# Kernel tuning notes

Hardware: AMD Instinct MI355X
Metric: run time of the kernel (lower is better)

## Reference

```python
import jax, jax.numpy as jnp
import numpy as np

P = 16                     # patch size
D = 192                    # embed dim (forced by SAT d_model=192)
NHEAD = 3                  # ViT-Tiny heads
SAT_H, SAT_DK, SAT_DV = 8, 32, 32
N_SLICE = 10
PER_LI = jnp.linspace(0.1, 1.0, N_SLICE)
LN_EPS = 1e-5


def layernorm(z, g, b):
    m = z.mean(-1, keepdims=True)
    v = ((z - m) ** 2).mean(-1, keepdims=True)
    return (z - m) * jax.lax.rsqrt(v + LN_EPS) * g + b


def setup_inputs() -> dict:
    key = jax.random.key(0)
    ks = jax.random.split(key, 32)
    B, IMG, DEPTH, MLP = 128, 224, 12, 4 * D
    S = (IMG // P) ** 2 + 1  # 197 tokens
    n = lambda k, sh: jax.random.normal(k, sh, jnp.float32) * 0.02
    z = lambda sh: jnp.zeros(sh, jnp.float32)
    o = lambda sh: jnp.ones(sh, jnp.float32)
    return {
        "x": jax.random.uniform(ks[0], (B, 3, IMG, IMG), jnp.float32),
        "x_g_norm": jax.random.uniform(ks[1], (B, 1, 56, 56), jnp.float32),
        "patch_w": n(ks[2], (D, 3, P, P)), "patch_b": z((D,)),
        "cls_token": n(ks[3], (1, 1, D)), "pos_embed": n(ks[4], (1, S, D)),
        "eleva_embed": n(ks[5], (1, D)),
        "sat_wq": n(ks[6], (D, SAT_H * SAT_DK)), "sat_bq": z((SAT_H * SAT_DK,)),
        "sat_wk": n(ks[7], (D, SAT_H * SAT_DK)), "sat_bk": z((SAT_H * SAT_DK,)),
        "sat_wv": n(ks[8], (D, SAT_H * SAT_DV)), "sat_bv": z((SAT_H * SAT_DV,)),
        "sat_wo": n(ks[9], (SAT_H * SAT_DV, D)), "sat_bo": z((D,)),
        "ln1_g": o((DEPTH, D)), "ln1_b": z((DEPTH, D)),
        "qkv_w": n(ks[10], (DEPTH, D, 3 * D)), "qkv_b": z((DEPTH, 3 * D)),
        "proj_w": n(ks[11], (DEPTH, D, D)), "proj_b": z((DEPTH, D)),
        "ln2_g": o((DEPTH, D)), "ln2_b": z((DEPTH, D)),
        "fc1_w": n(ks[12], (DEPTH, D, MLP)), "fc1_b": z((DEPTH, MLP)),
        "fc2_w": n(ks[13], (DEPTH, MLP, D)), "fc2_b": z((DEPTH, D)),
        "norm_g": o((D,)), "norm_b": z((D,)),
    }


def _forward(x, x_g_norm, patch_w, patch_b, cls_token, pos_embed, eleva_embed,
             sat_wq, sat_bq, sat_wk, sat_bk, sat_wv, sat_bv, sat_wo, sat_bo,
             ln1_g, ln1_b, qkv_w, qkv_b, proj_w, proj_b, ln2_g, ln2_b,
             fc1_w, fc1_b, fc2_w, fc2_b, norm_g, norm_b):
    B = x.shape[0]
    # --- patch embed: Conv2d(3, D, kernel=P, stride=P) -> [B, N, D] ---
    feat = jax.lax.conv_general_dilated(
        x, patch_w, (P, P), 'VALID', dimension_numbers=('NCHW', 'OIHW', 'NCHW'))
    feat = feat + patch_b[None, :, None, None]
    tokens = feat.reshape(B, D, -1).transpose(0, 2, 1)          # [B, 196, D]
    tok = jnp.concatenate([jnp.broadcast_to(cls_token, (B, 1, D)), tokens], axis=1)
    tok = tok + pos_embed                                        # [B, S, D]
    S = tok.shape[1]
    # --- elevation weight per sample (vectorized bisect + linear interp) ---
    means = x_g_norm.mean(axis=(1, 2, 3))                        # [B]
    idx = jnp.clip(jnp.searchsorted(PER_LI, means, side='left'), 0, N_SLICE - 1)
    per_hi = PER_LI[idx]
    per_lo = jnp.where(idx == 0, 0.0, PER_LI[jnp.maximum(idx - 1, 0)])
    idx_f = idx.astype(jnp.float32)
    idx_inter = idx_f - (per_hi - means) / (per_hi - per_lo)
    w = jnp.where(idx == N_SLICE - 1, idx_f, idx_inter) / N_SLICE  # [B]
    # --- SAT fusion: per (batch, token) a 2-element attention over (token, ele) ---
    ele = jnp.broadcast_to(eleva_embed[0] * w[:, None, None], tok.shape)  # [B,S,D]
    at_in = jnp.stack([tok, ele], axis=2)                        # [B, S, 2, D]
    q = (at_in @ sat_wq + sat_bq).reshape(B, S, 2, SAT_H, SAT_DK)
    k = (at_in @ sat_wk + sat_bk).reshape(B, S, 2, SAT_H, SAT_DK)
    v = (at_in @ sat_wv + sat_bv).reshape(B, S, 2, SAT_H, SAT_DV)
    att = jnp.einsum('bsqhd,bskhd->bshqk', q, k) * (1.0 / np.sqrt(SAT_DK))
    att = jax.nn.softmax(att, axis=-1)
    sat_o = jnp.einsum('bshqk,bskhd->bsqhd', att, v).reshape(B, S, 2, SAT_H * SAT_DV)
    sat_o = sat_o @ sat_wo + sat_bo                              # [B, S, 2, D]
    h = sat_o[..., 0, :] + sat_o[..., 1, :]                      # [B, S, D]
    # --- ViT blocks via scan over stacked layer params ---
    hd = D // NHEAD

    def block(z, p):
        l1g, l1b, qw, qb, pw, pb, l2g, l2b, f1w, f1b, f2w, f2b = p
        y = layernorm(z, l1g, l1b)
        qkv = y @ qw + qb                                        # [B, S, 3D]
        q_, k_, v_ = jnp.split(qkv, 3, axis=-1)
        q_ = q_.reshape(B, S, NHEAD, hd)
        k_ = k_.reshape(B, S, NHEAD, hd)
        v_ = v_.reshape(B, S, NHEAD, hd)
        a = jnp.einsum('bqhd,bkhd->bhqk', q_, k_) * (hd ** -0.5)
        a = jax.nn.softmax(a, axis=-1)
        o = jnp.einsum('bhqk,bkhd->bqhd', a, v_).reshape(B, S, D)
        z = z + o @ pw + pb
        y = layernorm(z, l2g, l2b)
        z = z + jax.nn.gelu(y @ f1w + f1b, approximate=False) @ f2w + f2b
        return z, None

    h, _ = jax.lax.scan(block, h, (ln1_g, ln1_b, qkv_w, qkv_b, proj_w, proj_b,
                                   ln2_g, ln2_b, fc1_w, fc1_b, fc2_w, fc2_b))
    h = layernorm(h, norm_g, norm_b)
    return h[:, 0]                                               # [B, D] cls token


def reference(x, x_g_norm, patch_w, patch_b, cls_token, pos_embed, eleva_embed,
              sat_wq, sat_bq, sat_wk, sat_bk, sat_wv, sat_bv, sat_wo, sat_bo,
              ln1_g, ln1_b, qkv_w, qkv_b, proj_w, proj_b, ln2_g, ln2_b,
              fc1_w, fc1_b, fc2_w, fc2_b, norm_g, norm_b):
    return _forward(x, x_g_norm, patch_w, patch_b, cls_token, pos_embed, eleva_embed,
                    sat_wq, sat_bq, sat_wk, sat_bk, sat_wv, sat_bv, sat_wo, sat_bo,
                    ln1_g, ln1_b, qkv_w, qkv_b, proj_w, proj_b, ln2_g, ln2_b,
                    fc1_w, fc1_b, fc2_w, fc2_b, norm_g, norm_b)
```

## Files before the change

### kernel.cpp

```cpp
#include <hip/hip_runtime.h>


#define BATCH 128
#define SEQ 197
#define BS_ROWS (BATCH * SEQ)
#define DMODEL 192
#define NPATCH 196
#define MROWS_PATCH (BATCH * NPATCH)
#define KPATCH 768
#define MLPDIM 768
#define DEPTH 12
#define SPAD 224

typedef float f32x4 __attribute__((ext_vector_type(4)));
typedef short s16x8 __attribute__((ext_vector_type(8)));

__device__ __forceinline__ float wredSum(float v) {
#pragma unroll
  for (int o = 32; o > 0; o >>= 1) v += __shfl_xor(v, o, 64);
  return v;
}

__device__ __forceinline__ unsigned short f2bf(float f) {
  union { float f; unsigned u; } v;
  v.f = f;
  unsigned r = v.u + 0x7FFFu + ((v.u >> 16) & 1u);
  return (unsigned short)(r >> 16);
}
__device__ __forceinline__ float bf2f(unsigned short u) {
  union { unsigned u; float f; } v;
  v.u = ((unsigned)u) << 16;
  return v.f;
}

__global__ __launch_bounds__(256) void eleva_w_kernel(const float* __restrict__ xg,
                                                      float* __restrict__ wout) {
  const int b = blockIdx.x;
  const float* p = xg + (size_t)b * 3136;
  float s = 0.f;
  for (int i = threadIdx.x; i < 3136; i += 256) s += p[i];
  __shared__ float partial[4];
  s = wredSum(s);
  if ((threadIdx.x & 63) == 0) partial[threadIdx.x >> 6] = s;
  __syncthreads();
  if (threadIdx.x == 0) {
    float m = (partial[0] + partial[1] + partial[2] + partial[3]) / 3136.f;
    int idx = 0;
#pragma unroll
    for (int i = 0; i < 10; i++) {
      float pv = 0.1f * (float)(i + 1);
      if (pv < m) idx = i + 1;
    }
    if (idx > 9) idx = 9;
    float wv;
    if (idx == 9) {
      wv = 9.f;
    } else {
      float hi = 0.1f * (float)(idx + 1);
      float lo = (idx == 0) ? 0.f : 0.1f * (float)idx;
      wv = (float)idx - (hi - m) / (hi - lo);
    }
    wout[b] = wv / 10.f;
  }
}

__global__ __launch_bounds__(256) void wtrans_kernel(const float* __restrict__ in,
                                                     unsigned short* __restrict__ out,
                                                     int R, int C) {
  const int z = blockIdx.z;
  in += (size_t)z * R * C;
  out += (size_t)z * R * C;
  const int c0 = blockIdx.x * 32, r0 = blockIdx.y * 32;
  __shared__ float t[32][33];
  const int tr = threadIdx.x >> 3, tc = (threadIdx.x & 7) * 4;
  const float4 v = *(const float4*)(in + (size_t)(r0 + tr) * C + c0 + tc);
  t[tr][tc] = v.x; t[tr][tc + 1] = v.y; t[tr][tc + 2] = v.z; t[tr][tc + 3] = v.w;
  __syncthreads();
  ushort4 o;
  o.x = f2bf(t[tc + 0][tr]);
  o.y = f2bf(t[tc + 1][tr]);
  o.z = f2bf(t[tc + 2][tr]);
  o.w = f2bf(t[tc + 3][tr]);
  *(ushort4*)(out + (size_t)(c0 + tr) * R + r0 + tc) = o;
}

__global__ __launch_bounds__(256) void convert_kernel(const float* __restrict__ in,
                                                      unsigned short* __restrict__ out, int n4) {
  const int i = blockIdx.x * 256 + threadIdx.x;
  if (i >= n4) return;
  const float4 v = *(const float4*)(in + (size_t)i * 4);
  ushort4 o;
  o.x = f2bf(v.x); o.y = f2bf(v.y); o.z = f2bf(v.z); o.w = f2bf(v.w);
  *(ushort4*)(out + (size_t)i * 4) = o;
}

__global__ __launch_bounds__(256) void im2col_kernel(const float* __restrict__ x,
                                                     unsigned short* __restrict__ col) {
  const int i = blockIdx.x * 256 + threadIdx.x;
  if (i >= MROWS_PATCH * KPATCH) return;
  const int k = i % KPATCH, row = i / KPATCH;
  const int b = row / NPATCH, p = row % NPATCH;
  const int py = p / 14, px = p % 14;
  const int c = k >> 8, r = (k >> 4) & 15, cc = k & 15;
  col[i] = f2bf(x[(((size_t)b * 3 + c) * 224 + (py * 16 + r)) * 224 + (px * 16 + cc)]);
}

__global__ __launch_bounds__(256) void assemble_kernel(const unsigned short* __restrict__ tok_raw,
                                                       const float* __restrict__ cls,
                                                       const float* __restrict__ pos,
                                                       float* __restrict__ H,
                                                       unsigned short* __restrict__ Hbf) {
  const int i = blockIdx.x * 256 + threadIdx.x;
  if (i >= BS_ROWS * DMODEL) return;
  const int d = i % DMODEL, row = i / DMODEL;
  const int b = row / SEQ, s = row % SEQ;
  float v;
  if (s == 0)
    v = cls[d] + pos[d];
  else
    v = bf2f(tok_raw[(size_t)(b * NPATCH + s - 1) * DMODEL + d]) + pos[(size_t)s * DMODEL + d];
  H[i] = v;
  Hbf[i] = f2bf(v);
}

__global__ __launch_bounds__(256) void ele_proj_kernel(
    const float* __restrict__ ele_emb, const float* __restrict__ wq, const float* __restrict__ bq,
    const float* __restrict__ wk, const float* __restrict__ bk,
    const float* __restrict__ wv, const float* __restrict__ bv,
    const float* __restrict__ wvec, float* __restrict__ eq, float* __restrict__ ek,
    float* __restrict__ ev) {
  const int b = blockIdx.x, t = threadIdx.x;
  __shared__ float es[DMODEL];
  if (t < DMODEL) es[t] = ele_emb[t] * wvec[b];
  __syncthreads();
  float aq = bq[t], ak = bk[t], av = bv[t];
  for (int d = 0; d < DMODEL; d++) {
    const float e = es[d];
    aq += e * wq[d * 256 + t];
    ak += e * wk[d * 256 + t];
    av += e * wv[d * 256 + t];
  }
  eq[b * 256 + t] = aq;
  ek[b * 256 + t] = ak;
  ev[b * 256 + t] = av;
}

__global__ __launch_bounds__(256) void sat_mix_kernel(
    const unsigned short* __restrict__ qt, const unsigned short* __restrict__ kt,
    const unsigned short* __restrict__ vt, const float* __restrict__ eq,
    const float* __restrict__ ek, const float* __restrict__ ev,
    unsigned short* __restrict__ o256) {
  const int gid = blockIdx.x * 256 + threadIdx.x;
  const int tok = gid >> 3, h = gid & 7;
  if (tok >= BS_ROWS) return;
  const int b = tok / SEQ;
  const unsigned short* qp = qt + (size_t)tok * 256 + h * 32;
  const unsigned short* kp = kt + (size_t)tok * 256 + h * 32;
  const unsigned short* vp = vt + (size_t)tok * 256 + h * 32;
  const float* eqp = eq + b * 256 + h * 32;
  const float* ekp = ek + b * 256 + h * 32;
  const float* evp = ev + b * 256 + h * 32;
  float s00 = 0.f, s01 = 0.f, s10 = 0.f, s11 = 0.f;
#pragma unroll 8
  for (int d = 0; d < 32; d++) {
    const float q_ = bf2f(qp[d]), k_ = bf2f(kp[d]), eq_ = eqp[d], ek_ = ekp[d];
    s00 += q_ * k_;
    s01 += q_ * ek_;
    s10 += eq_ * k_;
    s11 += eq_ * ek_;
  }
  const float sc = 0.17677669529663687f;
  s00 *= sc; s01 *= sc; s10 *= sc; s11 *= sc;
  const float m0 = fmaxf(s00, s01), m1 = fmaxf(s10, s11);
  const float e00 = __expf(s00 - m0), e01 = __expf(s01 - m0);
  const float e10 = __expf(s10 - m1), e11 = __expf(s11 - m1);
  const float w0 = e00 / (e00 + e01) + e10 / (e10 + e11);
  const float w1 = e01 / (e00 + e01) + e11 / (e10 + e11);
  unsigned short* op = o256 + (size_t)tok * 256 + h * 32;
#pragma unroll 8
  for (int d = 0; d < 32; d++) op[d] = f2bf(w0 * bf2f(vp[d]) + w1 * evp[d]);
}

template <int BK, int EPI>
__global__ __launch_bounds__(256) void gemm_mfma(const unsigned short* __restrict__ A,
                                                 const unsigned short* __restrict__ Bt,
                                                 const float* __restrict__ bias,
                                                 const float* __restrict__ res,
                                                 void* __restrict__ Cout, int M, int N, int K) {
  constexpr int SLOTS = BK / 8;
  __shared__ unsigned short As[128 * BK];
  __shared__ unsigned short Bs[64 * BK];
  const int tid = threadIdx.x, lane = tid & 63, w = tid >> 6;
  const int n0 = blockIdx.x * 64;
  const int m0 = blockIdx.y * 128;
  const int c = lane & 15, g = lane >> 4;
  const int wm = (w >> 1) * 64, wn = (w & 1) * 32;
  f32x4 acc[4][2] = {};
  for (int k0 = 0; k0 < K; k0 += BK) {
    if (k0) __syncthreads();
    constexpr int AI = 32 * SLOTS / 64;
#pragma unroll
    for (int it = 0; it < AI; it++) {
      const int s = it * 64 + lane;
      const int r = w * 32 + s / SLOTS;
      const int col = s % SLOTS;
      const int scol = col ^ (r & 7);
      const unsigned short* gp = A + (size_t)(m0 + r) * K + k0 + scol * 8;
      __builtin_amdgcn_global_load_lds(
          (const __attribute__((address_space(1))) unsigned int*)gp,
          (__attribute__((address_space(3))) unsigned int*)(As + ((size_t)(w * 32) * SLOTS + it * 64) * 8),
          16, 0, 0);
    }
    constexpr int BI = 16 * SLOTS / 64;
#pragma unroll
    for (int it = 0; it < BI; it++) {
      const int s = it * 64 + lane;
      const int r = w * 16 + s / SLOTS;
      const int col = s % SLOTS;
      const int scol = col ^ (r & 7);
      const unsigned short* gp = Bt + (size_t)(n0 + r) * K + k0 + scol * 8;
      __builtin_amdgcn_global_load_lds(
          (const __attribute__((address_space(1))) unsigned int*)gp,
          (__attribute__((address_space(3))) unsigned int*)(Bs + ((size_t)(w * 16) * SLOTS + it * 64) * 8),
          16, 0, 0);
    }
    __syncthreads();
#pragma unroll
    for (int kk = 0; kk < BK / 32; kk++) {
      const int sw = ((kk * 4 + g) ^ (c & 7)) << 3;
      s16x8 af[4], bfr[2];
#pragma unroll
      for (int i = 0; i < 4; i++) af[i] = *(const s16x8*)&As[(wm + i * 16 + c) * BK + sw];
#pragma unroll
      for (int j = 0; j < 2; j++) bfr[j] = *(const s16x8*)&Bs[(wn + j * 16 + c) * BK + sw];
#pragma unroll
      for (int i = 0; i < 4; i++)
#pragma unroll
        for (int j = 0; j < 2; j++)
          acc[i][j] = __builtin_amdgcn_mfma_f32_16x16x32_bf16(af[i], bfr[j], acc[i][j], 0, 0, 0);
    }
  }
  const int ncol0 = n0 + wn + c;
  float b0 = bias[ncol0], b1 = bias[ncol0 + 16];
  if (EPI == 3) { b0 *= 2.f; b1 *= 2.f; }
#pragma unroll
  for (int i = 0; i < 4; i++) {
#pragma unroll
    for (int r_ = 0; r_ < 4; r_++) {
      const size_t m = m0 + wm + i * 16 + g * 4 + r_;
#pragma unroll
      for (int j = 0; j < 2; j++) {
        float v = acc[i][j][r_] + (j ? b1 : b0);
        const size_t idx = m * N + ncol0 + j * 16;
        if (EPI == 0) {
          ((unsigned short*)Cout)[idx] = f2bf(v);
        } else if (EPI == 1) {
          v = 0.5f * v * (1.0f + erff(v * 0.70710678118654752f));
          ((unsigned short*)Cout)[idx] = f2bf(v);
        } else if (EPI == 2) {
          ((float*)Cout)[idx] = v + res[idx];
        } else {
          ((float*)Cout)[idx] = v;
        }
      }
    }
  }
}

__global__ __launch_bounds__(256) void ln_kernel(const float* __restrict__ X,
                                                 const float* __restrict__ g,
                                                 const float* __restrict__ bta,
                                                 unsigned short* __restrict__ Y, int nrows) {
  const int w = threadIdx.x >> 6, lane = threadIdx.x & 63;
  const int row = blockIdx.x * 4 + w;
  if (row >= nrows) return;
  const float* x = X + (size_t)row * DMODEL;
  const float x0 = x[lane], x1 = x[lane + 64], x2 = x[lane + 128];
  const float m = wredSum(x0 + x1 + x2) * (1.f / 192.f);
  const float d0 = x0 - m, d1 = x1 - m, d2 = x2 - m;
  const float v = wredSum(d0 * d0 + d1 * d1 + d2 * d2) * (1.f / 192.f);
  const float inv = rsqrtf(v + 1e-5f);
  unsigned short* y = Y + (size_t)row * DMODEL;
  y[lane] = f2bf(d0 * inv * g[lane] + bta[lane]);
  y[lane + 64] = f2bf(d1 * inv * g[lane + 64] + bta[lane + 64]);
  y[lane + 128] = f2bf(d2 * inv * g[lane + 128] + bta[lane + 128]);
}

__global__ __launch_bounds__(256) void final_ln_kernel(const float* __restrict__ H,
                                                       const float* __restrict__ g,
                                                       const float* __restrict__ bta,
                                                       float* __restrict__ out) {
  const int w = threadIdx.x >> 6, lane = threadIdx.x & 63;
  const int bi = blockIdx.x * 4 + w;
  if (bi >= BATCH) return;
  const float* x = H + (size_t)bi * SEQ * DMODEL;
  const float x0 = x[lane], x1 = x[lane + 64], x2 = x[lane + 128];
  const float m = wredSum(x0 + x1 + x2) * (1.f / 192.f);
  const float d0 = x0 - m, d1 = x1 - m, d2 = x2 - m;
  const float v = wredSum(d0 * d0 + d1 * d1 + d2 * d2) * (1.f / 192.f);
  const float inv = rsqrtf(v + 1e-5f);
  float* y = out + (size_t)bi * DMODEL;
  y[lane] = d0 * inv * g[lane] + bta[lane];
  y[lane + 64] = d1 * inv * g[lane + 64] + bta[lane + 64];
  y[lane + 128] = d2 * inv * g[lane + 128] + bta[lane + 128];
}

__global__ __launch_bounds__(256) void vtrans_kernel(const unsigned short* __restrict__ qkv,
                                                     unsigned short* __restrict__ vt) {
  const int bid = blockIdx.x;
  const int sc = bid & 3, bh = bid >> 2;
  const int b = bh / 3, h = bh % 3;
  const int s0 = sc * 64;
  __shared__ unsigned short t[64][72];
  const int tid = threadIdx.x;
  for (int e = tid; e < 64 * 64; e += 256) {
    const int sp = e >> 6, d = e & 63;
    const int s = s0 + sp;
    t[sp][d] = (s < SEQ) ? qkv[((size_t)(b * SEQ + s)) * 576 + 384 + h * 64 + d] : (unsigned short)0;
  }
  __syncthreads();
  for (int e = tid; e < 64 * 64; e += 256) {
    const int d = e >> 6, sp = e & 63;
    const int s = s0 + sp;
    if (s < SPAD) vt[((size_t)bh * 64 + d) * SPAD + s] = t[sp][d];
  }
}

__global__ __launch_bounds__(64) void attn_mfma_kernel(const unsigned short* __restrict__ qkv,
                                                       const unsigned short* __restrict__ vt,
                                                       unsigned short* __restrict__ out) {
  const int bid = blockIdx.x;
  const int bh = bid / 13, qt = bid % 13;
  const int b = bh / 3, h = bh % 3;
  const int row0 = b * SEQ;
  const int q0 = qt * 16;
  const int lane = threadIdx.x;
  const int c = lane & 15, g = lane >> 4;

  __shared__ __attribute__((aligned(16))) unsigned short P[16][232];

  const int qr = row0 + min(q0 + c, SEQ - 1);
  const unsigned short* qp = qkv + (size_t)qr * 576 + h * 64 + g * 8;
  const s16x8 qlo = *(const s16x8*)qp;
  const s16x8 qhi = *(const s16x8*)(qp + 32);

  f32x4 acc[13];
#pragma unroll
  for (int t = 0; t < 13; t++) {
    const int kr = row0 + min(t * 16 + c, SEQ - 1);
    const unsigned short* kp = qkv + (size_t)kr * 576 + 192 + h * 64 + g * 8;
    const s16x8 klo = *(const s16x8*)kp;
    const s16x8 khi = *(const s16x8*)(kp + 32);
    f32x4 z = {0.f, 0.f, 0.f, 0.f};
    z = __builtin_amdgcn_mfma_f32_16x16x32_bf16(qlo, klo, z, 0, 0, 0);
    acc[t] = __builtin_amdgcn_mfma_f32_16x16x32_bf16(qhi, khi, z, 0, 0, 0);
  }

  const bool m12 = (c >= 5);
#pragma unroll
  for (int r = 0; r < 4; r++) {
    float mx = -INFINITY;
#pragma unroll
    for (int t = 0; t < 13; t++) {
      const float v = (t == 12 && m12) ? -INFINITY : acc[t][r];
      mx = fmaxf(mx, v);
    }
#pragma unroll
    for (int o = 1; o <= 8; o <<= 1) mx = fmaxf(mx, __shfl_xor(mx, o, 64));
    const float ms = mx * 0.125f;
    float sum = 0.f;
#pragma unroll
    for (int t = 0; t < 13; t++) {
      const float e = (t == 12 && m12) ? 0.f : __expf(acc[t][r] * 0.125f - ms);
      acc[t][r] = e;
      sum += e;
    }
#pragma unroll
    for (int o = 1; o <= 8; o <<= 1) sum += __shfl_xor(sum, o, 64);
    const float inv = 1.f / sum;
#pragma unroll
    for (int t = 0; t < 13; t++) P[g * 4 + r][t * 16 + c] = f2bf(acc[t][r] * inv);
  }
  {
    unsigned short z4[4] = {0, 0, 0, 0};
    *(uint2*)&P[c][208 + g * 4] = *(uint2*)z4;
  }
  __builtin_amdgcn_s_waitcnt(0);

  f32x4 oacc[4];
#pragma unroll
  for (int dt = 0; dt < 4; dt++) oacc[dt] = (f32x4){0.f, 0.f, 0.f, 0.f};
  const unsigned short* vbase = vt + (size_t)bh * 64 * SPAD;
#pragma unroll
  for (int ch = 0; ch < 7; ch++) {
    const s16x8 pa = *(const s16x8*)&P[c][ch * 32 + g * 8];
#pragma unroll
    for (int dt = 0; dt < 4; dt++) {
      const s16x8 vb = *(const s16x8*)(vbase + (size_t)(dt * 16 + c) * SPAD + ch * 32 + g * 8);
      oacc[dt] = __builtin_amdgcn_mfma_f32_16x16x32_bf16(pa, vb, oacc[dt], 0, 0, 0);
    }
  }

#pragma unroll
  for (int dt = 0; dt < 4; dt++) {
#pragma unroll
    for (int r = 0; r < 4; r++) {
      const int q = q0 + g * 4 + r;
      if (q < SEQ) out[(size_t)(row0 + q) * DMODEL + h * 64 + dt * 16 + c] = f2bf(oacc[dt][r]);
    }
  }
}

extern "C" void kernel_launch(void* const* d_in, const int* in_sizes, int n_in,
                              void* d_out, int out_size, void* d_ws, size_t ws_size,
                              hipStream_t stream) {
  const float* x       = (const float*)d_in[0];
  const float* xg      = (const float*)d_in[1];
  const float* patch_w = (const float*)d_in[2];
  const float* patch_b = (const float*)d_in[3];
  const float* cls_tok = (const float*)d_in[4];
  const float* pos_emb = (const float*)d_in[5];
  const float* ele_emb = (const float*)d_in[6];
  const float* sat_wq  = (const float*)d_in[7];
  const float* sat_bq  = (const float*)d_in[8];
  const float* sat_wk  = (const float*)d_in[9];
  const float* sat_bk  = (const float*)d_in[10];
  const float* sat_wv  = (const float*)d_in[11];
  const float* sat_bv  = (const float*)d_in[12];
  const float* sat_wo  = (const float*)d_in[13];
  const float* sat_bo  = (const float*)d_in[14];
  const float* ln1_g   = (const float*)d_in[15];
  const float* ln1_b   = (const float*)d_in[16];
  const float* qkv_w   = (const float*)d_in[17];
  const float* qkv_b   = (const float*)d_in[18];
  const float* proj_w  = (const float*)d_in[19];
  const float* proj_b  = (const float*)d_in[20];
  const float* ln2_g   = (const float*)d_in[21];
  const float* ln2_b   = (const float*)d_in[22];
  const float* fc1_w   = (const float*)d_in[23];
  const float* fc1_b   = (const float*)d_in[24];
  const float* fc2_w   = (const float*)d_in[25];
  const float* fc2_b   = (const float*)d_in[26];
  const float* norm_g  = (const float*)d_in[27];
  const float* norm_b  = (const float*)d_in[28];
  float* out = (float*)d_out;
  float* ws = (float*)d_ws;

  float* W_ELE = ws;
  float* EQ = ws + 256;
  float* EK = EQ + 32768;
  float* EV = EK + 32768;
  float* H = ws + 98560;
  unsigned short* Hbf   = (unsigned short*)(ws + 4940032);
  unsigned short* Ybf   = (unsigned short*)(ws + 7360768);
  unsigned short* QKVbf = (unsigned short*)(ws + 9781504);
  unsigned short* MLPbf = (unsigned short*)(ws + 17043712);
  unsigned short* VTB   = (unsigned short*)(ws + 26726656);
  unsigned short* WTS   = (unsigned short*)(ws + 29479168);

  unsigned short* qkv_wt   = WTS;
  unsigned short* proj_wt  = WTS + 1327104;
  unsigned short* fc1_wt   = WTS + 1769472;
  unsigned short* fc2_wt   = WTS + 3538944;
  unsigned short* patch_bf = WTS + 5308416;
  unsigned short* satq_t   = WTS + 5455872;
  unsigned short* satk_t   = WTS + 5505024;
  unsigned short* satv_t   = WTS + 5554176;
  unsigned short* sato_t   = WTS + 5603328;

  unsigned short* COLbf  = MLPbf;
  unsigned short* TOKRAW = Ybf;
  unsigned short* QTbf   = QKVbf;
  unsigned short* KTbf   = QKVbf + 6455296;
  unsigned short* VTbf   = MLPbf;
  unsigned short* O256bf = MLPbf + 6455296;

  wtrans_kernel<<<dim3(18, 6, 12), 256, 0, stream>>>(qkv_w, qkv_wt, 192, 576);
  wtrans_kernel<<<dim3(6, 6, 12), 256, 0, stream>>>(proj_w, proj_wt, 192, 192);
  wtrans_kernel<<<dim3(24, 6, 12), 256, 0, stream>>>(fc1_w, fc1_wt, 192, 768);
  wtrans_kernel<<<dim3(6, 24, 12), 256, 0, stream>>>(fc2_w, fc2_wt, 768, 192);
  wtrans_kernel<<<dim3(8, 6, 1), 256, 0, stream>>>(sat_wq, satq_t, 192, 256);
  wtrans_kernel<<<dim3(8, 6, 1), 256, 0, stream>>>(sat_wk, satk_t, 192, 256);
  wtrans_kernel<<<dim3(8, 6, 1), 256, 0, stream>>>(sat_wv, satv_t, 192, 256);
  wtrans_kernel<<<dim3(6, 8, 1), 256, 0, stream>>>(sat_wo, sato_t, 256, 192);
  convert_kernel<<<144, 256, 0, stream>>>(patch_w, patch_bf, 36864);

  eleva_w_kernel<<<BATCH, 256, 0, stream>>>(xg, W_ELE);

  im2col_kernel<<<(MROWS_PATCH * KPATCH) / 256, 256, 0, stream>>>(x, COLbf);
  gemm_mfma<192, 0><<<dim3(3, 196), 256, 0, stream>>>(COLbf, patch_bf, patch_b, nullptr,
                                                      TOKRAW, MROWS_PATCH, DMODEL, KPATCH);
  assemble_kernel<<<(BS_ROWS * DMODEL) / 256, 256, 0, stream>>>(TOKRAW, cls_tok, pos_emb, H, Hbf);

  ele_proj_kernel<<<BATCH, 256, 0, stream>>>(ele_emb, sat_wq, sat_bq, sat_wk, sat_bk,
                                             sat_wv, sat_bv, W_ELE, EQ, EK, EV);
  gemm_mfma<192, 0><<<dim3(4, 197), 256, 0, stream>>>(Hbf, satq_t, sat_bq, nullptr, QTbf,
                                                      BS_ROWS, 256, DMODEL);
  gemm_mfma<192, 0><<<dim3(4, 197), 256, 0, stream>>>(Hbf, satk_t, sat_bk, nullptr, KTbf,
                                                      BS_ROWS, 256, DMODEL);
  gemm_mfma<192, 0><<<dim3(4, 197), 256, 0, stream>>>(Hbf, satv_t, sat_bv, nullptr, VTbf,
                                                      BS_ROWS, 256, DMODEL);
  sat_mix_kernel<<<BS_ROWS / 32, 256, 0, stream>>>(QTbf, KTbf, VTbf, EQ, EK, EV, O256bf);
  gemm_mfma<128, 3><<<dim3(3, 197), 256, 0, stream>>>(O256bf, sato_t, sat_bo, nullptr, H,
                                                      BS_ROWS, DMODEL, 256);

  for (int l = 0; l < DEPTH; l++) {
    ln_kernel<<<BS_ROWS / 4, 256, 0, stream>>>(H, ln1_g + l * DMODEL, ln1_b + l * DMODEL, Ybf,
                                               BS_ROWS);
    gemm_mfma<192, 0><<<dim3(9, 197), 256, 0, stream>>>(
        Ybf, qkv_wt + (size_t)l * 110592, qkv_b + l * 576, nullptr, QKVbf, BS_ROWS, 576, DMODEL);
    vtrans_kernel<<<BATCH * 3 * 4, 256, 0, stream>>>(QKVbf, VTB);
    attn_mfma_kernel<<<BATCH * 3 * 13, 64, 0, stream>>>(QKVbf, VTB, Ybf);
    gemm_mfma<192, 2><<<dim3(3, 197), 256, 0, stream>>>(
        Ybf, proj_wt + (size_t)l * 36864, proj_b + l * DMODEL, H, H, BS_ROWS, DMODEL, DMODEL);
    ln_kernel<<<BS_ROWS / 4, 256, 0, stream>>>(H, ln2_g + l * DMODEL, ln2_b + l * DMODEL, Ybf,
                                               BS_ROWS);
    gemm_mfma<192, 1><<<dim3(12, 197), 256, 0, stream>>>(
        Ybf, fc1_wt + (size_t)l * 147456, fc1_b + l * MLPDIM, nullptr, MLPbf, BS_ROWS, MLPDIM,
        DMODEL);
    gemm_mfma<192, 2><<<dim3(3, 197), 256, 0, stream>>>(
        MLPbf, fc2_wt + (size_t)l * 147456, fc2_b + l * DMODEL, H, H, BS_ROWS, DMODEL, MLPDIM);
  }

  final_ln_kernel<<<BATCH / 4, 256, 0, stream>>>(H, norm_g, norm_b, out);
}
```

Before: 2.011 ms.

## Double-buffer GEMM with 128x96 tiles, fuse SAT QKV and patch assembly

The MFMA GEMM now uses BK=64 with two LDS buffers, so the next K-slice loads while the current one computes. Tiles widen from 64 to 96 columns, which changes every grid shape. The three SAT Q/K/V projections are merged into one N=768 GEMM with concatenated weights and biases. The patch-embed GEMM epilogue writes H and Hbf with positional embedding added directly, replacing assemble_kernel with a small cls_kernel. im2col is vectorised to 8 elements per thread. These changes cut kernel launches, intermediate traffic and LDS stalls, at the cost of more LDS per block, which may reduce occupancy.

```diff
diff --git a/kernel.cpp b/kernel.cpp
--- a/kernel.cpp
+++ b/kernel.cpp
@@ -97,30 +97,33 @@
 __global__ __launch_bounds__(256) void im2col_kernel(const float* __restrict__ x,
                                                      unsigned short* __restrict__ col) {
   const int i = blockIdx.x * 256 + threadIdx.x;
-  if (i >= MROWS_PATCH * KPATCH) return;
-  const int k = i % KPATCH, row = i / KPATCH;
+  if (i >= MROWS_PATCH * KPATCH / 8) return;
+  const int k = (i % 96) * 8, row = i / 96;
   const int b = row / NPATCH, p = row % NPATCH;
   const int py = p / 14, px = p % 14;
   const int c = k >> 8, r = (k >> 4) & 15, cc = k & 15;
-  col[i] = f2bf(x[(((size_t)b * 3 + c) * 224 + (py * 16 + r)) * 224 + (px * 16 + cc)]);
-}
-
-__global__ __launch_bounds__(256) void assemble_kernel(const unsigned short* __restrict__ tok_raw,
-                                                       const float* __restrict__ cls,
-                                                       const float* __restrict__ pos,
-                                                       float* __restrict__ H,
-                                                       unsigned short* __restrict__ Hbf) {
+  const float* src = x + (((size_t)b * 3 + c) * 224 + (py * 16 + r)) * 224 + (px * 16 + cc);
+  const float4 v0 = *(const float4*)src;
+  const float4 v1 = *(const float4*)(src + 4);
+  s16x8 o;
+  o[0] = (short)f2bf(v0.x); o[1] = (short)f2bf(v0.y);
+  o[2] = (short)f2bf(v0.z); o[3] = (short)f2bf(v0.w);
+  o[4] = (short)f2bf(v1.x); o[5] = (short)f2bf(v1.y);
+  o[6] = (short)f2bf(v1.z); o[7] = (short)f2bf(v1.w);
+  *(s16x8*)(col + (size_t)i * 8) = o;
+}
+
+__global__ __launch_bounds__(256) void cls_kernel(const float* __restrict__ cls,
+                                                  const float* __restrict__ pos,
+                                                  float* __restrict__ H,
+                                                  unsigned short* __restrict__ Hbf) {
   const int i = blockIdx.x * 256 + threadIdx.x;
-  if (i >= BS_ROWS * DMODEL) return;
-  const int d = i % DMODEL, row = i / DMODEL;
-  const int b = row / SEQ, s = row % SEQ;
-  float v;
-  if (s == 0)
-    v = cls[d] + pos[d];
-  else
-    v = bf2f(tok_raw[(size_t)(b * NPATCH + s - 1) * DMODEL + d]) + pos[(size_t)s * DMODEL + d];
-  H[i] = v;
-  Hbf[i] = f2bf(v);
+  if (i >= BATCH * DMODEL) return;
+  const int b = i / DMODEL, d = i % DMODEL;
+  const float v = cls[d] + pos[d];
+  const size_t idx = (size_t)b * SEQ * DMODEL + d;
+  H[idx] = v;
+  Hbf[idx] = f2bf(v);
 }
 
 __global__ __launch_bounds__(256) void ele_proj_kernel(
@@ -128,8 +131,13 @@
     const float* __restrict__ wk, const float* __restrict__ bk,
     const float* __restrict__ wv, const float* __restrict__ bv,
     const float* __restrict__ wvec, float* __restrict__ eq, float* __restrict__ ek,
-    float* __restrict__ ev) {
+    float* __restrict__ ev, float* __restrict__ satb) {
   const int b = blockIdx.x, t = threadIdx.x;
+  if (b == 0) {
+    satb[t] = bq[t];
+    satb[256 + t] = bk[t];
+    satb[512 + t] = bv[t];
+  }
   __shared__ float es[DMODEL];
   if (t < DMODEL) es[t] = ele_emb[t] * wvec[b];
   __syncthreads();
@@ -146,17 +154,16 @@
 }
 
 __global__ __launch_bounds__(256) void sat_mix_kernel(
-    const unsigned short* __restrict__ qt, const unsigned short* __restrict__ kt,
-    const unsigned short* __restrict__ vt, const float* __restrict__ eq,
+    const unsigned short* __restrict__ qkv768, const float* __restrict__ eq,
     const float* __restrict__ ek, const float* __restrict__ ev,
     unsigned short* __restrict__ o256) {
   const int gid = blockIdx.x * 256 + threadIdx.x;
   const int tok = gid >> 3, h = gid & 7;
   if (tok >= BS_ROWS) return;
   const int b = tok / SEQ;
-  const unsigned short* qp = qt + (size_t)tok * 256 + h * 32;
-  const unsigned short* kp = kt + (size_t)tok * 256 + h * 32;
-  const unsigned short* vp = vt + (size_t)tok * 256 + h * 32;
+  const unsigned short* qp = qkv768 + (size_t)tok * 768 + h * 32;
+  const unsigned short* kp = qp + 256;
+  const unsigned short* vp = qp + 512;
   const float* eqp = eq + b * 256 + h * 32;
   const float* ekp = ek + b * 256 + h * 32;
   const float* evp = ev + b * 256 + h * 32;
@@ -181,86 +188,115 @@
   for (int d = 0; d < 32; d++) op[d] = f2bf(w0 * bf2f(vp[d]) + w1 * evp[d]);
 }
 
-template <int BK, int EPI>
+template <int EPI>
 __global__ __launch_bounds__(256) void gemm_mfma(const unsigned short* __restrict__ A,
                                                  const unsigned short* __restrict__ Bt,
                                                  const float* __restrict__ bias,
                                                  const float* __restrict__ res,
-                                                 void* __restrict__ Cout, int M, int N, int K) {
-  constexpr int SLOTS = BK / 8;
-  __shared__ unsigned short As[128 * BK];
-  __shared__ unsigned short Bs[64 * BK];
+                                                 void* __restrict__ Cout,
+                                                 unsigned short* __restrict__ aux_hbf,
+                                                 const float* __restrict__ aux_pos,
+                                                 int M, int N, int K) {
+  __shared__ unsigned short As[2 * 128 * 64];
+  __shared__ unsigned short Bs[2 * 96 * 64];
   const int tid = threadIdx.x, lane = tid & 63, w = tid >> 6;
-  const int n0 = blockIdx.x * 64;
+  const int n0 = blockIdx.x * 96;
   const int m0 = blockIdx.y * 128;
   const int c = lane & 15, g = lane >> 4;
-  const int wm = (w >> 1) * 64, wn = (w & 1) * 32;
-  f32x4 acc[4][2] = {};
-  for (int k0 = 0; k0 < K; k0 += BK) {
-    if (k0) __syncthreads();
-    constexpr int AI = 32 * SLOTS / 64;
-#pragma unroll
-    for (int it = 0; it < AI; it++) {
+  const int wm = (w >> 1) * 64, wn = (w & 1) * 48;
+  f32x4 acc[4][3] = {};
+
+  auto stage = [&](int k0, int buf) {
+#pragma unroll
+    for (int it = 0; it < 4; it++) {
       const int s = it * 64 + lane;
-      const int r = w * 32 + s / SLOTS;
-      const int col = s % SLOTS;
-      const int scol = col ^ (r & 7);
+      const int r = w * 32 + (s >> 3);
+      const int scol = (s & 7) ^ (r & 7);
       const unsigned short* gp = A + (size_t)(m0 + r) * K + k0 + scol * 8;
       __builtin_amdgcn_global_load_lds(
           (const __attribute__((address_space(1))) unsigned int*)gp,
-          (__attribute__((address_space(3))) unsigned int*)(As + ((size_t)(w * 32) * SLOTS + it * 64) * 8),
+          (__attribute__((address_space(3))) unsigned int*)(As + buf * 8192 + w * 2048 + it * 512),
           16, 0, 0);
     }
-    constexpr int BI = 16 * SLOTS / 64;
-#pragma unroll
-    for (int it = 0; it < BI; it++) {
+#pragma unroll
+    for (int it = 0; it < 3; it++) {
       const int s = it * 64 + lane;
-      const int r = w * 16 + s / SLOTS;
-      const int col = s % SLOTS;
-      const int scol = col ^ (r & 7);
+      const int r = w * 24 + (s >> 3);
+      const int scol = (s & 7) ^ (r & 7);
       const unsigned short* gp = Bt + (size_t)(n0 + r) * K + k0 + scol * 8;
       __builtin_amdgcn_global_load_lds(
           (const __attribute__((address_space(1))) unsigned int*)gp,
-          (__attribute__((address_space(3))) unsigned int*)(Bs + ((size_t)(w * 16) * SLOTS + it * 64) * 8),
+          (__attribute__((address_space(3))) unsigned int*)(Bs + buf * 6144 + w * 1536 + it * 512),
           16, 0, 0);
     }
+  };
+
+  auto compute = [&](int buf) {
+#pragma unroll
+    for (int kk = 0; kk < 2; kk++) {
+      const int sw = (((kk * 4 + g) ^ (c & 7))) << 3;
+      s16x8 af[4], bfr[3];
+#pragma unroll
+      for (int i = 0; i < 4; i++)
+        af[i] = *(const s16x8*)&As[buf * 8192 + (wm + i * 16 + c) * 64 + sw];
+#pragma unroll
+      for (int j = 0; j < 3; j++)
+        bfr[j] = *(const s16x8*)&Bs[buf * 6144 + (wn + j * 16 + c) * 64 + sw];
+#pragma unroll
+      for (int i = 0; i < 4; i++)
+#pragma unroll
+        for (int j = 0; j < 3; j++)
+          acc[i][j] = __builtin_amdgcn_mfma_f32_16x16x32_bf16(af[i], bfr[j], acc[i][j], 0, 0, 0);
+    }
+  };
+
+  int cur = 0;
+  stage(0, 0);
+  __syncthreads();
+  for (int k0 = 64; k0 < K; k0 += 64) {
+    stage(k0, cur ^ 1);
+    compute(cur);
     __syncthreads();
-#pragma unroll
-    for (int kk = 0; kk < BK / 32; kk++) {
-      const int sw = ((kk * 4 + g) ^ (c & 7)) << 3;
-      s16x8 af[4], bfr[2];
-#pragma unroll
-      for (int i = 0; i < 4; i++) af[i] = *(const s16x8*)&As[(wm + i * 16 + c) * BK + sw];
-#pragma unroll
-      for (int j = 0; j < 2; j++) bfr[j] = *(const s16x8*)&Bs[(wn + j * 16 + c) * BK + sw];
-#pragma unroll
-      for (int i = 0; i < 4; i++)
-#pragma unroll
-        for (int j = 0; j < 2; j++)
-          acc[i][j] = __builtin_amdgcn_mfma_f32_16x16x32_bf16(af[i], bfr[j], acc[i][j], 0, 0, 0);
-    }
-  }
+    cur ^= 1;
+  }
+  compute(cur);
+
   const int ncol0 = n0 + wn + c;
-  float b0 = bias[ncol0], b1 = bias[ncol0 + 16];
-  if (EPI == 3) { b0 *= 2.f; b1 *= 2.f; }
+  float bv[3];
+#pragma unroll
+  for (int j = 0; j < 3; j++) bv[j] = bias[ncol0 + j * 16] * (EPI == 3 ? 2.f : 1.f);
 #pragma unroll
   for (int i = 0; i < 4; i++) {
 #pragma unroll
     for (int r_ = 0; r_ < 4; r_++) {
-      const size_t m = m0 + wm + i * 16 + g * 4 + r_;
-#pragma unroll
-      for (int j = 0; j < 2; j++) {
-        float v = acc[i][j][r_] + (j ? b1 : b0);
-        const size_t idx = m * N + ncol0 + j * 16;
-        if (EPI == 0) {
-          ((unsigned short*)Cout)[idx] = f2bf(v);
-        } else if (EPI == 1) {
-          v = 0.5f * v * (1.0f + erff(v * 0.70710678118654752f));
-          ((unsigned short*)Cout)[idx] = f2bf(v);
-        } else if (EPI == 2) {
-          ((float*)Cout)[idx] = v + res[idx];
-        } else {
+      const int mrow = m0 + wm + i * 16 + g * 4 + r_;
+      if (EPI == 4) {
+        const int bb = mrow / 196;
+        const int p = mrow - bb * 196;
+        const size_t drow = (size_t)mrow + bb + 1;
+#pragma unroll
+        for (int j = 0; j < 3; j++) {
+          const int col = ncol0 + j * 16;
+          const float v = acc[i][j][r_] + bv[j] + aux_pos[(size_t)(p + 1) * DMODEL + col];
+          const size_t idx = drow * DMODEL + col;
           ((float*)Cout)[idx] = v;
+          aux_hbf[idx] = f2bf(v);
+        }
+      } else {
+#pragma unroll
+        for (int j = 0; j < 3; j++) {
+          float v = acc[i][j][r_] + bv[j];
+          const size_t idx = (size_t)mrow * N + ncol0 + j * 16;
+          if (EPI == 0) {
+            ((unsigned short*)Cout)[idx] = f2bf(v);
+          } else if (EPI == 1) {
+            v = 0.5f * v * (1.0f + erff(v * 0.70710678118654752f));
+            ((unsigned short*)Cout)[idx] = f2bf(v);
+          } else if (EPI == 2) {
+            ((float*)Cout)[idx] = v + res[idx];
+          } else {
+            ((float*)Cout)[idx] = v;
+          }
         }
       }
     }
@@ -457,69 +493,64 @@
   unsigned short* MLPbf = (unsigned short*)(ws + 17043712);
   unsigned short* VTB   = (unsigned short*)(ws + 26726656);
   unsigned short* WTS   = (unsigned short*)(ws + 29479168);
+  float* SATB = ws + 32305408;
 
   unsigned short* qkv_wt   = WTS;
   unsigned short* proj_wt  = WTS + 1327104;
   unsigned short* fc1_wt   = WTS + 1769472;
   unsigned short* fc2_wt   = WTS + 3538944;
   unsigned short* patch_bf = WTS + 5308416;
-  unsigned short* satq_t   = WTS + 5455872;
-  unsigned short* satk_t   = WTS + 5505024;
-  unsigned short* satv_t   = WTS + 5554176;
+  unsigned short* satqkv_t = WTS + 5455872;
   unsigned short* sato_t   = WTS + 5603328;
 
-  unsigned short* COLbf  = MLPbf;
-  unsigned short* TOKRAW = Ybf;
-  unsigned short* QTbf   = QKVbf;
-  unsigned short* KTbf   = QKVbf + 6455296;
-  unsigned short* VTbf   = MLPbf;
-  unsigned short* O256bf = MLPbf + 6455296;
+  unsigned short* COLbf   = MLPbf;
+  unsigned short* SATQKV  = MLPbf;
+  unsigned short* O256bf  = QKVbf;
 
   wtrans_kernel<<<dim3(18, 6, 12), 256, 0, stream>>>(qkv_w, qkv_wt, 192, 576);
   wtrans_kernel<<<dim3(6, 6, 12), 256, 0, stream>>>(proj_w, proj_wt, 192, 192);
   wtrans_kernel<<<dim3(24, 6, 12), 256, 0, stream>>>(fc1_w, fc1_wt, 192, 768);
   wtrans_kernel<<<dim3(6, 24, 12), 256, 0, stream>>>(fc2_w, fc2_wt, 768, 192);
-  wtrans_kernel<<<dim3(8, 6, 1), 256, 0, stream>>>(sat_wq, satq_t, 192, 256);
-  wtrans_kernel<<<dim3(8, 6, 1), 256, 0, stream>>>(sat_wk, satk_t, 192, 256);
-  wtrans_kernel<<<dim3(8, 6, 1), 256, 0, stream>>>(sat_wv, satv_t, 192, 256);
+  wtrans_kernel<<<dim3(8, 6, 1), 256, 0, stream>>>(sat_wq, satqkv_t, 192, 256);
+  wtrans_kernel<<<dim3(8, 6, 1), 256, 0, stream>>>(sat_wk, satqkv_t + 49152, 192, 256);
+  wtrans_kernel<<<dim3(8, 6, 1), 256, 0, stream>>>(sat_wv, satqkv_t + 98304, 192, 256);
   wtrans_kernel<<<dim3(6, 8, 1), 256, 0, stream>>>(sat_wo, sato_t, 256, 192);
   convert_kernel<<<144, 256, 0, stream>>>(patch_w, patch_bf, 36864);
 
   eleva_w_kernel<<<BATCH, 256, 0, stream>>>(xg, W_ELE);
 
-  im2col_kernel<<<(MROWS_PATCH * KPATCH) / 256, 256, 0, stream>>>(x, COLbf);
-  gemm_mfma<192, 0><<<dim3(3, 196), 256, 0, stream>>>(COLbf, patch_bf, patch_b, nullptr,
-                                                      TOKRAW, MROWS_PATCH, DMODEL, KPATCH);
-  assemble_kernel<<<(BS_ROWS * DMODEL) / 256, 256, 0, stream>>>(TOKRAW, cls_tok, pos_emb, H, Hbf);
+  im2col_kernel<<<(MROWS_PATCH * KPATCH / 8) / 256, 256, 0, stream>>>(x, COLbf);
+  gemm_mfma<4><<<dim3(2, 196), 256, 0, stream>>>(COLbf, patch_bf, patch_b, nullptr, H, Hbf,
+                                                 pos_emb, MROWS_PATCH, DMODEL, KPATCH);
+  cls_kernel<<<(BATCH * DMODEL) / 256, 256, 0, stream>>>(cls_tok, pos_emb, H, Hbf);
 
   ele_proj_kernel<<<BATCH, 256, 0, stream>>>(ele_emb, sat_wq, sat_bq, sat_wk, sat_bk,
-                                             sat_wv, sat_bv, W_ELE, EQ, EK, EV);
-  gemm_mfma<192, 0><<<dim3(4, 197), 256, 0, stream>>>(Hbf, satq_t, sat_bq, nullptr, QTbf,
-                                                      BS_ROWS, 256, DMODEL);
-  gemm_mfma<192, 0><<<dim3(4, 197), 256, 0, stream>>>(Hbf, satk_t, sat_bk, nullptr, KTbf,
-                                                      BS_ROWS, 256, DMODEL);
-  gemm_mfma<192, 0><<<dim3(4, 197), 256, 0, stream>>>(Hbf, satv_t, sat_bv, nullptr, VTbf,
-                                                      BS_ROWS, 256, DMODEL);
-  sat_mix_kernel<<<BS_ROWS / 32, 256, 0, stream>>>(QTbf, KTbf, VTbf, EQ, EK, EV, O256bf);
-  gemm_mfma<128, 3><<<dim3(3, 197), 256, 0, stream>>>(O256bf, sato_t, sat_bo, nullptr, H,
-                                                      BS_ROWS, DMODEL, 256);
+                                             sat_wv, sat_bv, W_ELE, EQ, EK, EV, SATB);
+  gemm_mfma<0><<<dim3(8, 197), 256, 0, stream>>>(Hbf, satqkv_t, SATB, nullptr, SATQKV,
+                                                 nullptr, nullptr, BS_ROWS, 768, DMODEL);
+  sat_mix_kernel<<<BS_ROWS / 32, 256, 0, stream>>>(SATQKV, EQ, EK, EV, O256bf);
+  gemm_mfma<3><<<dim3(2, 197), 256, 0, stream>>>(O256bf, sato_t, sat_bo, nullptr, H,
+                                                 nullptr, nullptr, BS_ROWS, DMODEL, 256);
 
   for (int l = 0; l < DEPTH; l++) {
     ln_kernel<<<BS_ROWS / 4, 256, 0, stream>>>(H, ln1_g + l * DMODEL, ln1_b + l * DMODEL, Ybf,
                                                BS_ROWS);
-    gemm_mfma<192, 0><<<dim3(9, 197), 256, 0, stream>>>(
-        Ybf, qkv_wt + (size_t)l * 110592, qkv_b + l * 576, nullptr, QKVbf, BS_ROWS, 576, DMODEL);
+    gemm_mfma<0><<<dim3(6, 197), 256, 0, stream>>>(Ybf, qkv_wt + (size_t)l * 110592,
+                                                   qkv_b + l * 576, nullptr, QKVbf, nullptr,
+                                                   nullptr, BS_ROWS, 576, DMODEL);
     vtrans_kernel<<<BATCH * 3 * 4, 256, 0, stream>>>(QKVbf, VTB);
     attn_mfma_kernel<<<BATCH * 3 * 13, 64, 0, stream>>>(QKVbf, VTB, Ybf);
-    gemm_mfma<192, 2><<<dim3(3, 197), 256, 0, stream>>>(
-        Ybf, proj_wt + (size_t)l * 36864, proj_b + l * DMODEL, H, H, BS_ROWS, DMODEL, DMODEL);
+    gemm_mfma<2><<<dim3(2, 197), 256, 0, stream>>>(Ybf, proj_wt + (size_t)l * 36864,
+                                                   proj_b + l * DMODEL, H, H, nullptr, nullptr,
+                                                   BS_ROWS, DMODEL, DMODEL);
     ln_kernel<<<BS_ROWS / 4, 256, 0, stream>>>(H, ln2_g + l * DMODEL, ln2_b + l * DMODEL, Ybf,
                                                BS_ROWS);
-    gemm_mfma<192, 1><<<dim3(12, 197), 256, 0, stream>>>(
-        Ybf, fc1_wt + (size_t)l * 147456, fc1_b + l * MLPDIM, nullptr, MLPbf, BS_ROWS, MLPDIM,
-        DMODEL);
-    gemm_mfma<192, 2><<<dim3(3, 197), 256, 0, stream>>>(
-        MLPbf, fc2_wt + (size_t)l * 147456, fc2_b + l * DMODEL, H, H, BS_ROWS, DMODEL, MLPDIM);
+    gemm_mfma<1><<<dim3(8, 197), 256, 0, stream>>>(Ybf, fc1_wt + (size_t)l * 147456,
+                                                   fc1_b + l * MLPDIM, nullptr, MLPbf, nullptr,
+                                                   nullptr, BS_ROWS, MLPDIM, DMODEL);
+    gemm_mfma<2><<<dim3(2, 197), 256, 0, stream>>>(MLPbf, fc2_wt + (size_t)l * 147456,
+                                                   fc2_b + l * DMODEL, H, H, nullptr, nullptr,
+                                                   BS_ROWS, DMODEL, MLPDIM);
   }
 
   final_ln_kernel<<<BATCH / 4, 256, 0, stream>>>(H, norm_g, norm_b, out);
```

Measured after the change: 2.002 ms. No clear change (-0.5%).
